# Kernel optimization log

Hardware: AMD Instinct MI355X
Metric: run time of the kernel (lower is better)

The kernel has to match this reference:

```python
import jax, jax.numpy as jnp
import numpy as np

H, W = 512, 1024            # panorama resolution
GRID = 512                  # occupancy histogram resolution (height=width=512)
ABS_SCALE = 20000.0         # mm, ground-plane extent
UNIT_SCALE = 1000.0         # m -> mm
COUNT_TH = 100.0            # histogram count clamp


def _xyz_sphere(ref_plan):
    # Vectorized version of the original double loop.
    i = np.arange(H, dtype=np.float32)
    j = np.arange(W, dtype=np.float32)
    theta = -np.pi * (i / (H - 1) - 0.5)          # [H]
    phi = np.pi * (2.0 * j / (W - 1) - 1.0)       # [W]
    ct, st = np.cos(theta)[:, None], np.sin(theta)[:, None]   # [H,1]
    cp, sp = np.cos(phi)[None, :], np.sin(phi)[None, :]       # [1,W]
    if ref_plan == 'horizontal':
        P = np.stack([cp * ct, sp * ct, np.broadcast_to(st, (H, W))], 0)
    elif ref_plan == 'vertical':
        P = np.stack([cp * ct, np.broadcast_to(-st, (H, W)), sp * ct], 0)
    else:  # lateral
        P = np.stack([sp * ct, np.broadcast_to(-st, (H, W)), cp * ct], 0)
    return jnp.asarray(P.astype(np.float32))      # [3,H,W]

_SPHERES = [_xyz_sphere(p) for p in ('horizontal', 'vertical', 'lateral')]


def _density_one(depth_hw, sph):
    # depth_hw: [H,W]; sph: [3,H,W]
    ps = depth_hw[None] * sph                               # [3,H,W] 3D points
    xy = ps[:2].reshape(2, -1) * UNIT_SCALE                 # [2,N] mm, (x,y)
    coords = (xy + ABS_SCALE / 2.0) / ABS_SCALE * GRID      # [2,N] in grid units
    coords = jnp.clip(jnp.round(coords), 0.0, GRID - 1).astype(jnp.int32)
    flat = coords[1] * GRID + coords[0]                     # density[y, x]
    hist = jnp.zeros(GRID * GRID, jnp.float32).at[flat].add(1.0)
    hist = jnp.minimum(hist, COUNT_TH)
    hist = hist / jnp.max(hist)
    return hist.reshape(GRID, GRID)


def _density(depth, sph):
    # depth: [B,1,H,W] -> [B,GRID,GRID], batched scatter histogram
    return jax.vmap(_density_one, in_axes=(0, None))(depth[:, 0], sph)


def _inverse_huber(pred, gt):
    # berHu loss: L1 below c = 0.2*max|d|, scaled L2 above.
    diff = jnp.abs(pred - gt)
    c = 0.2 * jnp.max(diff)
    loss = jnp.where(diff <= c, diff, (diff * diff + c * c) / (2.0 * c))
    return jnp.mean(loss)


def setup_inputs() -> dict:
    key = jax.random.key(0)
    k1, k2 = jax.random.split(key)
    # indoor depths in [0, 10) meters so histogram bins are populated
    pred = jax.random.uniform(k1, (16, 1, H, W), jnp.float32) * 10.0
    gt = jax.random.uniform(k2, (16, 1, H, W), jnp.float32) * 10.0
    return {"pred_depth": pred, "gt_depth": gt}


def reference(pred_depth, gt_depth):
    total = jnp.float32(0.0)
    for sph in _SPHERES:  # fixed 3 projection planes
        pred_om = _density(pred_depth, sph)
        gt_om = _density(gt_depth, sph)
        total = total + _inverse_huber(pred_om, gt_om)
    return total
```

## Files before the change

kernel.cpp:

```cpp
#include <hip/hip_runtime.h>

#define PI_F 3.14159265358979323846f

#define MAXZ_OFF_B   24576
#define HIST_OFF_B   32768
#define BUCK_OFF_B   25198592
#define REGION_U16   12320

__device__ inline float div20000(float a) {
    const float r = 1.0f / 20000.0f;
    float q0 = a * r;
    float e = fmaf(-20000.0f, q0, a);
    return fmaf(e, r, q0);
}

__device__ inline int bin1(float v) {
    float f = rintf(div20000(v + 10000.0f) * 512.0f);
    return (int)fminf(fmaxf(f, 0.0f), 511.0f);
}

__global__ __launch_bounds__(256) void trig_kernel(
    float* __restrict__ tbl, unsigned* __restrict__ maxz,
    float* __restrict__ out) {
    const int t = threadIdx.x + blockIdx.x * 256;
    if (blockIdx.x == 0) {
        if (threadIdx.x < 128) maxz[threadIdx.x] = 0u;
        if (threadIdx.x == 128) out[0] = 0.0f;
    }
    if (t < 1024) {
        float fj = (float)t;
        float phi = PI_F * ((2.0f * fj) / 1023.0f - 1.0f);
        tbl[t] = cosf(phi);
        tbl[1024 + t] = sinf(phi);
    } else {
        int i = t - 1024;
        float fi = (float)i;
        float theta = -PI_F * (fi / 511.0f - 0.5f);
        tbl[2048 + i] = cosf(theta);
        tbl[2560 + i] = sinf(theta);
    }
}

__global__ __launch_bounds__(256) void bin_kernel(
    const float* __restrict__ pred, const float* __restrict__ gt,
    const float* __restrict__ tbl, unsigned short* __restrict__ buck) {
    __shared__ unsigned cnt[192];
    __shared__ unsigned bsum[24];
    __shared__ unsigned off[25];
    __shared__ __align__(16) unsigned short sdata[12288];
    const int tid = threadIdx.x, wg = blockIdx.x;
    const unsigned rep = (unsigned)(tid & 7);
    const int xcd = wg & 7, i4 = (wg >> 3) & 127, hh = wg >> 10;
    const int h = (hh << 3) | xcd;
    if (tid < 192) cnt[tid] = 0u;
    const float4 cp4 = *(const float4*)&tbl[tid << 2];
    const float4 sp4 = *(const float4*)&tbl[1024 + (tid << 2)];
    const float4 ct4 = *(const float4*)&tbl[2048 + (i4 << 2)];
    const float4 st4 = *(const float4*)&tbl[2560 + (i4 << 2)];
    __syncthreads();
    const float* img = ((h >> 4) ? gt : pred) + ((h & 15) << 19);
    unsigned items[48];
    #pragma unroll
    for (int r = 0; r < 4; ++r) {
        const int i = i4 * 4 + r;
        const float4 d4 = *(const float4*)(img + (i << 10) + (tid << 2));
        const float ct = (&ct4.x)[r], st = (&st4.x)[r];
        #pragma unroll
        for (int k = 0; k < 4; ++k) {
            float d = (&d4.x)[k];
            float aA = (&cp4.x)[k] * ct;
            float aB = (&sp4.x)[k] * ct;
            float A = (d * aA) * 1000.0f;
            float B = (d * aB) * 1000.0f;
            float C = (d * (-st)) * 1000.0f;
            int iA = bin1(A), iB = bin1(B), iC = bin1(C);
            unsigned f0 = ((unsigned)iB << 9) | (unsigned)iA;
            unsigned f1 = ((unsigned)iC << 9) | (unsigned)iA;
            unsigned f2 = ((unsigned)iC << 9) | (unsigned)iB;
            unsigned b0 = f0 >> 15;
            unsigned b1 = 8u + (f1 >> 15);
            unsigned b2 = 16u + (f2 >> 15);
            unsigned r0 = atomicAdd(&cnt[(b0 << 3) | rep], 1u);
            unsigned r1 = atomicAdd(&cnt[(b1 << 3) | rep], 1u);
            unsigned r2 = atomicAdd(&cnt[(b2 << 3) | rep], 1u);
            const int base = (r * 4 + k) * 3;
            items[base + 0] = (b0 << 27) | (rep << 24) | (r0 << 15) | (f0 & 32767u);
            items[base + 1] = (b1 << 27) | (rep << 24) | (r1 << 15) | (f1 & 32767u);
            items[base + 2] = (b2 << 27) | (rep << 24) | (r2 << 15) | (f2 & 32767u);
        }
    }
    __syncthreads();
    if (tid < 24) {
        unsigned s = 0;
        #pragma unroll
        for (int r = 0; r < 8; ++r) {
            unsigned t = cnt[(tid << 3) | r];
            cnt[(tid << 3) | r] = s;
            s += t;
        }
        bsum[tid] = s;
    }
    __syncthreads();
    if (tid == 0) {
        unsigned s = 0;
        #pragma unroll
        for (int b = 0; b < 24; ++b) { off[b] = s; s += bsum[b]; }
        off[24] = s;
    }
    __syncthreads();
    if (tid < 24) {
        unsigned o = off[tid];
        #pragma unroll
        for (int r = 0; r < 8; ++r) cnt[(tid << 3) | r] += o;
    }
    __syncthreads();
    #pragma unroll
    for (int t = 0; t < 48; ++t) {
        const unsigned it = items[t];
        const unsigned slot = ((it >> 27) << 3) | ((it >> 24) & 7u);
        sdata[cnt[slot] + ((it >> 15) & 511u)] = (unsigned short)(it & 32767u);
    }
    __syncthreads();
    unsigned short* regG = buck + (size_t)wg * REGION_U16;
    if (tid < 25) regG[tid] = (unsigned short)off[tid];
    const uint4* s4p = (const uint4*)sdata;
    uint4* g4 = (uint4*)(regG + 32);
    #pragma unroll
    for (int c = 0; c < 6; ++c) g4[(c << 8) + tid] = s4p[(c << 8) + tid];
}

__global__ __launch_bounds__(1024, 8) void scan_kernel(
    const unsigned short* __restrict__ buck, unsigned* __restrict__ hp,
    unsigned* __restrict__ maxraw) {
    __shared__ unsigned lh[16384];
    __shared__ unsigned s4[16];
    const int tid = threadIdx.x, wg = blockIdx.x;
    const int xcd = wg & 7, hhi = (wg >> 3) & 3;
    const int X = wg >> 5;
    const int pair = X / 6, idx6 = X % 6;
    const int plane = idx6 >> 1;
    const int band = (idx6 & 1) ? (4 + pair) : (3 - pair);
    const int h = (hhi << 3) | xcd;
    const int bucket = plane * 8 + band;

    #pragma unroll
    for (int k = 0; k < 4; ++k)
        *(uint4*)&lh[(k << 12) + (tid << 2)] = make_uint4(0, 0, 0, 0);
    __syncthreads();

    const int wid = tid >> 6, lane = tid & 63;
    for (int i4 = wid; i4 < 128; i4 += 16) {
        const unsigned short* reg =
            buck + (size_t)(xcd | (i4 << 3) | (hhi << 10)) * REGION_U16;
        const int lo = reg[bucket], hi = reg[bucket + 1];
        const unsigned short* data = reg + 32;
        int a = (lo + 7) & ~7;
        if (a > hi) a = hi;
        const int head = a - lo;
        if (lane < head) {
            const unsigned id = data[lo + lane];
            atomicAdd(&lh[id >> 1], 1u << ((id & 1u) << 4));
        }
        const int nv = (hi - a) >> 3;
        for (int v = lane; v < nv; v += 64) {
            const uint4 w = *(const uint4*)&data[a + (v << 3)];
            #pragma unroll
            for (int q = 0; q < 4; ++q) {
                const unsigned u = (&w.x)[q];
                const unsigned idl = u & 65535u, idh = u >> 16;
                atomicAdd(&lh[idl >> 1], 1u << ((idl & 1u) << 4));
                atomicAdd(&lh[idh >> 1], 1u << ((idh & 1u) << 4));
            }
        }
        const int tail = (hi - a) & 7;
        if (lane < tail) {
            const unsigned id = data[a + (nv << 3) + lane];
            atomicAdd(&lh[id >> 1], 1u << ((id & 1u) << 4));
        }
    }
    __syncthreads();

    unsigned m = 0;
    unsigned* gout = hp + ((plane * 32 + h) << 16) + (band << 13);
    #pragma unroll
    for (int k = 0; k < 8; ++k) {
        int w = (k << 10) + tid;
        unsigned v0 = lh[2 * w], v1 = lh[2 * w + 1];
        unsigned c0 = v0 & 65535u, c1 = v0 >> 16;
        unsigned c2 = v1 & 65535u, c3 = v1 >> 16;
        m = max(max(m, max(c0, c1)), max(c2, c3));
        gout[w] = min(c0, 255u) | (min(c1, 255u) << 8) |
                  (min(c2, 255u) << 16) | (min(c3, 255u) << 24);
    }
    #pragma unroll
    for (int o = 32; o; o >>= 1) m = max(m, (unsigned)__shfl_down((int)m, o));
    if ((tid & 63) == 0) s4[tid >> 6] = m;
    __syncthreads();
    if (tid == 0) {
        #pragma unroll
        for (int k = 1; k < 16; ++k) m = max(m, s4[k]);
        atomicMax(&maxraw[plane * 32 + h], m);
    }
}

__device__ inline float blockMaxF(float v) {
    #pragma unroll
    for (int o = 32; o; o >>= 1) v = fmaxf(v, __shfl_down(v, o));
    __shared__ float s[4];
    if ((threadIdx.x & 63) == 0) s[threadIdx.x >> 6] = v;
    __syncthreads();
    if (threadIdx.x == 0) v = fmaxf(fmaxf(s[0], s[1]), fmaxf(s[2], s[3]));
    return v;
}

__device__ inline float blockSumF(float v) {
    #pragma unroll
    for (int o = 32; o; o >>= 1) v += __shfl_down(v, o);
    __shared__ float s[4];
    if ((threadIdx.x & 63) == 0) s[threadIdx.x >> 6] = v;
    __syncthreads();
    if (threadIdx.x == 0) v = (s[0] + s[1]) + (s[2] + s[3]);
    return v;
}

__global__ void maxdiff_kernel(const unsigned* __restrict__ hp,
                               const unsigned* __restrict__ maxraw,
                               unsigned* __restrict__ maxdiff) {
    int blk = blockIdx.x;
    int b = blk & 15, chunk = (blk >> 4) & 15, plane = blk >> 8;
    const unsigned* P = hp + ((plane * 32 + b) << 16) + (chunk << 12);
    const unsigned* G = P + (16 << 16);
    float nP = fminf((float)maxraw[plane * 32 + b], 100.0f);
    float nG = fminf((float)maxraw[plane * 32 + 16 + b], 100.0f);
    float m = 0.0f;
    #pragma unroll
    for (int k = 0; k < 4; ++k) {
        uint4 wp = *(const uint4*)&P[(k << 10) + (threadIdx.x << 2)];
        uint4 wg = *(const uint4*)&G[(k << 10) + (threadIdx.x << 2)];
        #pragma unroll
        for (int w = 0; w < 4; ++w) {
            unsigned up = (&wp.x)[w], ug = (&wg.x)[w];
            #pragma unroll
            for (int s = 0; s < 32; s += 8) {
                float pn = fminf((float)((up >> s) & 255u), 100.0f) / nP;
                float gn = fminf((float)((ug >> s) & 255u), 100.0f) / nG;
                m = fmaxf(m, fabsf(pn - gn));
            }
        }
    }
    m = blockMaxF(m);
    if (threadIdx.x == 0) atomicMax(&maxdiff[plane], __float_as_uint(m));
}

__global__ void loss_kernel(const unsigned* __restrict__ hp,
                            const unsigned* __restrict__ maxraw,
                            const unsigned* __restrict__ maxdiff,
                            float* __restrict__ out) {
    int blk = blockIdx.x;
    int b = blk & 15, chunk = (blk >> 4) & 15, plane = blk >> 8;
    const unsigned* P = hp + ((plane * 32 + b) << 16) + (chunk << 12);
    const unsigned* G = P + (16 << 16);
    float c = 0.2f * __uint_as_float(maxdiff[plane]);
    float nP = fminf((float)maxraw[plane * 32 + b], 100.0f);
    float nG = fminf((float)maxraw[plane * 32 + 16 + b], 100.0f);
    float acc = 0.0f;
    #pragma unroll
    for (int k = 0; k < 4; ++k) {
        uint4 wp = *(const uint4*)&P[(k << 10) + (threadIdx.x << 2)];
        uint4 wg = *(const uint4*)&G[(k << 10) + (threadIdx.x << 2)];
        #pragma unroll
        for (int w = 0; w < 4; ++w) {
            unsigned up = (&wp.x)[w], ug = (&wg.x)[w];
            #pragma unroll
            for (int s = 0; s < 32; s += 8) {
                float pn = fminf((float)((up >> s) & 255u), 100.0f) / nP;
                float gn = fminf((float)((ug >> s) & 255u), 100.0f) / nG;
                float d = fabsf(pn - gn);
                acc += (d <= c) ? d : (d * d + c * c) / (2.0f * c);
            }
        }
    }
    acc = blockSumF(acc);
    if (threadIdx.x == 0) atomicAdd(out, acc / 4194304.0f);
}

extern "C" void kernel_launch(void* const* d_in, const int* in_sizes, int n_in,
                              void* d_out, int out_size, void* d_ws, size_t ws_size,
                              hipStream_t stream) {
    const float* pred = (const float*)d_in[0];
    const float* gt   = (const float*)d_in[1];
    float* out        = (float*)d_out;
    char* ws          = (char*)d_ws;

    float* tbl        = (float*)ws;
    unsigned* maxz    = (unsigned*)(ws + MAXZ_OFF_B);
    unsigned* maxraw  = maxz;
    unsigned* maxdiff = maxz + 96;
    unsigned* hp      = (unsigned*)(ws + HIST_OFF_B);
    unsigned short* buck = (unsigned short*)(ws + BUCK_OFF_B);

    trig_kernel<<<6, 256, 0, stream>>>(tbl, maxz, out);
    bin_kernel<<<4096, 256, 0, stream>>>(pred, gt, tbl, buck);
    scan_kernel<<<768, 1024, 0, stream>>>(buck, hp, maxraw);
    maxdiff_kernel<<<768, 256, 0, stream>>>(hp, maxraw, maxdiff);
    loss_kernel<<<768, 256, 0, stream>>>(hp, maxraw, maxdiff, out);
}
```

Measured before the change: 206.6 us.

## Collapse uniform-bin histogram atomics and use LDS normalization tables

In the shared-memory histogram scatter, each 8-element vector is checked for all-identical bin ids. When a whole wavefront holds the same bin, one lane issues a single aggregated atomic. When only one lane's vector is uniform, it issues one atomic of 8 instead of eight separate ones. This targets LDS atomic contention on heavily populated bins, at the cost of extra ballots and compares on every vector. The maxdiff and loss kernels also replace the per-element clamp and divide with a 256-entry LDS lookup table per block, adding a barrier and LDS reads in place of float divides.

```diff
diff --git a/kernel.cpp b/kernel.cpp
--- a/kernel.cpp
+++ b/kernel.cpp
@@ -164,12 +164,28 @@
         const int nv = (hi - a) >> 3;
         for (int v = lane; v < nv; v += 64) {
             const uint4 w = *(const uint4*)&data[a + (v << 3)];
-            #pragma unroll
-            for (int q = 0; q < 4; ++q) {
-                const unsigned u = (&w.x)[q];
-                const unsigned idl = u & 65535u, idh = u >> 16;
-                atomicAdd(&lh[idl >> 1], 1u << ((idl & 1u) << 4));
-                atomicAdd(&lh[idh >> 1], 1u << ((idh & 1u) << 4));
+            const bool uni = (w.x == w.y) && (w.y == w.z) && (w.z == w.w) &&
+                             ((w.x >> 16) == (w.x & 65535u));
+            const unsigned long long act = __ballot(1);
+            const unsigned first = __builtin_amdgcn_readfirstlane(w.x);
+            const unsigned long long same = __ballot(uni && (w.x == first));
+            if (same == act) {
+                if (lane == (int)(__ffsll(act) - 1)) {
+                    const unsigned id = first & 65535u;
+                    atomicAdd(&lh[id >> 1],
+                              (8u * (unsigned)__popcll(act)) << ((id & 1u) << 4));
+                }
+            } else if (uni) {
+                const unsigned id = w.x & 65535u;
+                atomicAdd(&lh[id >> 1], 8u << ((id & 1u) << 4));
+            } else {
+                #pragma unroll
+                for (int q = 0; q < 4; ++q) {
+                    const unsigned u = (&w.x)[q];
+                    const unsigned idl = u & 65535u, idh = u >> 16;
+                    atomicAdd(&lh[idl >> 1], 1u << ((idl & 1u) << 4));
+                    atomicAdd(&lh[idh >> 1], 1u << ((idh & 1u) << 4));
+                }
             }
         }
         const int tail = (hi - a) & 7;
@@ -226,24 +242,29 @@
 __global__ void maxdiff_kernel(const unsigned* __restrict__ hp,
                                const unsigned* __restrict__ maxraw,
                                unsigned* __restrict__ maxdiff) {
+    __shared__ float tP[256], tG[256];
     int blk = blockIdx.x;
     int b = blk & 15, chunk = (blk >> 4) & 15, plane = blk >> 8;
     const unsigned* P = hp + ((plane * 32 + b) << 16) + (chunk << 12);
     const unsigned* G = P + (16 << 16);
     float nP = fminf((float)maxraw[plane * 32 + b], 100.0f);
     float nG = fminf((float)maxraw[plane * 32 + 16 + b], 100.0f);
+    const int tid = threadIdx.x;
+    tP[tid] = fminf((float)tid, 100.0f) / nP;
+    tG[tid] = fminf((float)tid, 100.0f) / nG;
+    __syncthreads();
     float m = 0.0f;
     #pragma unroll
     for (int k = 0; k < 4; ++k) {
-        uint4 wp = *(const uint4*)&P[(k << 10) + (threadIdx.x << 2)];
-        uint4 wg = *(const uint4*)&G[(k << 10) + (threadIdx.x << 2)];
+        uint4 wp = *(const uint4*)&P[(k << 10) + (tid << 2)];
+        uint4 wg = *(const uint4*)&G[(k << 10) + (tid << 2)];
         #pragma unroll
         for (int w = 0; w < 4; ++w) {
             unsigned up = (&wp.x)[w], ug = (&wg.x)[w];
             #pragma unroll
             for (int s = 0; s < 32; s += 8) {
-                float pn = fminf((float)((up >> s) & 255u), 100.0f) / nP;
-                float gn = fminf((float)((ug >> s) & 255u), 100.0f) / nG;
+                float pn = tP[(up >> s) & 255u];
+                float gn = tG[(ug >> s) & 255u];
                 m = fmaxf(m, fabsf(pn - gn));
             }
         }
@@ -256,6 +277,7 @@
                             const unsigned* __restrict__ maxraw,
                             const unsigned* __restrict__ maxdiff,
                             float* __restrict__ out) {
+    __shared__ float tP[256], tG[256];
     int blk = blockIdx.x;
     int b = blk & 15, chunk = (blk >> 4) & 15, plane = blk >> 8;
     const unsigned* P = hp + ((plane * 32 + b) << 16) + (chunk << 12);
@@ -263,18 +285,22 @@
     float c = 0.2f * __uint_as_float(maxdiff[plane]);
     float nP = fminf((float)maxraw[plane * 32 + b], 100.0f);
     float nG = fminf((float)maxraw[plane * 32 + 16 + b], 100.0f);
+    const int tid = threadIdx.x;
+    tP[tid] = fminf((float)tid, 100.0f) / nP;
+    tG[tid] = fminf((float)tid, 100.0f) / nG;
+    __syncthreads();
     float acc = 0.0f;
     #pragma unroll
     for (int k = 0; k < 4; ++k) {
-        uint4 wp = *(const uint4*)&P[(k << 10) + (threadIdx.x << 2)];
-        uint4 wg = *(const uint4*)&G[(k << 10) + (threadIdx.x << 2)];
+        uint4 wp = *(const uint4*)&P[(k << 10) + (tid << 2)];
+        uint4 wg = *(const uint4*)&G[(k << 10) + (tid << 2)];
         #pragma unroll
         for (int w = 0; w < 4; ++w) {
             unsigned up = (&wp.x)[w], ug = (&wg.x)[w];
             #pragma unroll
             for (int s = 0; s < 32; s += 8) {
-                float pn = fminf((float)((up >> s) & 255u), 100.0f) / nP;
-                float gn = fminf((float)((ug >> s) & 255u), 100.0f) / nG;
+                float pn = tP[(up >> s) & 255u];
+                float gn = tG[(ug >> s) & 255u];
                 float d = fabsf(pn - gn);
                 acc += (d <= c) ? d : (d * d + c * c) / (2.0f * c);
             }
```

New measurement: 211.3 us. 2.3% more time.
